# Optimization experiments

Measured on AMD Instinct MI355X. Metric: run time of the kernel, lower is better.

Reference implementation:

```python
import jax, jax.numpy as jnp
import numpy as np
from jax import lax

EPS = 1e-05
Q = 4          # window size (hard-coded in BotBlock)
HEADS = 4
DIM = 16       # bottleneck(64) // heads(4)


def conv3x3(x, w, b):
    # x: [N,C,H,W], w: [O,I,3,3]
    y = lax.conv_general_dilated(x, w, (1, 1), ((1, 1), (1, 1)),
                                 dimension_numbers=('NCHW', 'OIHW', 'NCHW'))
    return y + b[None, :, None, None]


def batchnorm(x, gamma, beta):
    # training-mode BN: batch statistics over (N,H,W), biased variance
    m = jnp.mean(x, axis=(0, 2, 3), keepdims=True)
    v = jnp.var(x, axis=(0, 2, 3), keepdims=True)
    xn = (x - m) * lax.rsqrt(v + EPS)
    return xn * gamma[None, :, None, None] + beta[None, :, None, None]


def rel_to_abs(x):
    # x: [B, H, L, 2L-1] -> [B, H, L, L] via pad/reshape trick
    B, H, L, _ = x.shape
    x = jnp.pad(x, ((0, 0), (0, 0), (0, 0), (0, 1)))          # [B,H,L,2L]
    flat = x.reshape(B, H, -1)                                  # [B,H,2L*L]
    flat = jnp.pad(flat, ((0, 0), (0, 0), (0, L - 1)))
    final = flat.reshape(B, H, L + 1, 2 * L - 1)
    return final[:, :, :L, L - 1:]                              # [B,H,L,L]


def relative_logits_1d(q, rel_k, perm):
    # q: [b, n, h, w, d], rel_k: [2w-1, d]
    b, n, h, w, d = q.shape
    rl = jnp.einsum('bnhwd,md->bnhwm', q, rel_k)
    rl = rl.reshape(b, n * h, w, 2 * w - 1)
    rl = rel_to_abs(rl)                                         # [b, n*h, w, w]
    rl = rl.reshape(b, n, h, w, w)
    rl = jnp.broadcast_to(rl[:, :, :, None], (b, n, h, h, w, w))
    return jnp.transpose(rl, perm)


def rel_pos_attention(q, k, v, rel_w, rel_h):
    # q,k,v: [b, heads, h, w, d]
    b, n, h, w, d = q.shape
    q = q * (d ** -0.5)
    logits = jnp.einsum('bnhwd,bnpqd->bnhwpq', q, k)
    logits = logits + relative_logits_1d(q, rel_w, (0, 1, 2, 4, 3, 5))
    logits = logits + relative_logits_1d(jnp.transpose(q, (0, 1, 3, 2, 4)),
                                         rel_h, (0, 1, 4, 2, 5, 3))
    weights = jax.nn.softmax(logits.reshape(b, n, h, w, h * w), axis=-1)
    weights = weights.reshape(b, n, h, w, h, w)
    out = jnp.einsum('bnhwpq,bnpqd->bhwnd', weights, v)         # [b,h,w,n,d]
    return out.reshape(b, h, w, n * d)                          # fold heads


def setup_inputs() -> dict:
    key = jax.random.key(0)
    ks = jax.random.split(key, 16)
    C_in, C_bot, C_out = 64, 64, 256
    inp = {
        'x': jax.random.normal(ks[0], (2, C_in, 256, 256), jnp.float32),
        'conv1_w': jax.random.normal(ks[1], (C_bot, C_in, 3, 3), jnp.float32) * 0.05,
        'conv1_b': jnp.zeros((C_bot,), jnp.float32),
        'bn1_g': jnp.ones((C_bot,), jnp.float32),
        'bn1_b': jnp.zeros((C_bot,), jnp.float32),
        'wq': jax.random.normal(ks[2], (C_bot, HEADS, DIM), jnp.float32) * 0.01,
        'wk': jax.random.normal(ks[3], (C_bot, HEADS, DIM), jnp.float32) * 0.01,
        'wv': jax.random.normal(ks[4], (C_bot, HEADS, DIM), jnp.float32) * 0.01,
        'rel_w': jax.random.normal(ks[5], (2 * Q - 1, DIM), jnp.float32) * (DIM ** -0.5),
        'rel_h': jax.random.normal(ks[6], (2 * Q - 1, DIM), jnp.float32) * (DIM ** -0.5),
        'bn2_g': jnp.ones((C_bot,), jnp.float32),
        'bn2_b': jnp.zeros((C_bot,), jnp.float32),
        'conv3_w': jax.random.normal(ks[7], (C_out, C_bot, 3, 3), jnp.float32) * 0.05,
        'conv3_b': jnp.zeros((C_out,), jnp.float32),
        # NOTE: original init_zero=True zeros bn3 gamma; we randomize it so the
        # output (and gradients) are non-trivial for kernel correctness checks.
        'bn3_g': jax.random.normal(ks[8], (C_out,), jnp.float32),
        'bn3_b': jnp.zeros((C_out,), jnp.float32),
    }
    return inp


def reference(x, conv1_w, conv1_b, bn1_g, bn1_b, wq, wk, wv, rel_w, rel_h,
              bn2_g, bn2_b, conv3_w, conv3_b, bn3_g, bn3_b):
    N, C, H, W = x.shape
    P_h, P_w = H // Q, W // Q
    # raw memory reinterpretation into 4x4 blocks (matches torch .reshape)
    xb = x.reshape(N * P_h * P_w, C, Q, Q)
    out = jax.nn.relu(batchnorm(conv3x3(xb, conv1_w, conv1_b), bn1_g, bn1_b))
    # GroupPointWise projections: NCHW -> NHWC then einsum
    feat = jnp.transpose(out, (0, 2, 3, 1))                     # [b,h,w,c]
    q = jnp.einsum('bhwc,cnp->bnhwp', feat, wq)
    k = jnp.einsum('bhwc,cnp->bnhwp', feat, wk)
    v = jnp.einsum('bhwc,cnp->bnhwp', feat, wv)
    o = rel_pos_attention(q, k, v, rel_w, rel_h)                # [b,h,w,c]
    o = jnp.transpose(o, (0, 3, 1, 2))                          # NCHW
    o = jax.nn.relu(batchnorm(o, bn2_g, bn2_b))
    o = batchnorm(conv3x3(o, conv3_w, conv3_b), bn3_g, bn3_b)   # no act
    C1 = o.shape[1]
    o = o.reshape(N, C1, H, W)
    return jax.nn.relu(o)
```

## Files before the change

### kernel.cpp

```cpp
#include <hip/hip_runtime.h>
#include <stdint.h>


#define EPSV 1e-5f
#define INV_N (1.0f / 131072.0f)

typedef unsigned short u16;
typedef __attribute__((ext_vector_type(8))) short short8b;
typedef __attribute__((ext_vector_type(4))) short short4b;
typedef __attribute__((ext_vector_type(4))) float f32x4;

__device__ __forceinline__ u16 f2bf(float f) {
  unsigned u = __float_as_uint(f);
  u += 0x7fffu + ((u >> 16) & 1u);
  return (u16)(u >> 16);
}
__device__ __forceinline__ float bf2f(u16 h) {
  return __uint_as_float((unsigned)h << 16);
}
__device__ __forceinline__ unsigned cvtpk(float lo, float hi) {
  unsigned r;
  asm("v_cvt_pk_bf16_f32 %0, %1, %2" : "=v"(r) : "v"(lo), "v"(hi));
  return r;
}
__device__ __forceinline__ short4b pack4(unsigned lo, unsigned hi) {
  union { unsigned u[2]; short4b s; } x;
  x.u[0] = lo; x.u[1] = hi;
  return x.s;
}
__device__ __forceinline__ f32x4 mfma16(short4b a, short4b b, f32x4 c) {
#if __has_builtin(__builtin_amdgcn_mfma_f32_16x16x16_bf16)
  return __builtin_amdgcn_mfma_f32_16x16x16_bf16(a, b, c, 0, 0, 0);
#elif __has_builtin(__builtin_amdgcn_mfma_f32_16x16x16bf16_1k)
  return __builtin_amdgcn_mfma_f32_16x16x16bf16_1k(a, b, c, 0, 0, 0);
#else
  f32x4 d;
  asm volatile("v_mfma_f32_16x16x16_bf16 %0, %1, %2, %3\n\ts_nop 7\n\ts_nop 7"
               : "=v"(d) : "v"(a), "v"(b), "v"(c));
  return d;
#endif
}

__device__ __forceinline__ float bn_scale(const float* __restrict__ acc,
                                          const float* __restrict__ gam,
                                          const float* __restrict__ bet,
                                          int C, int c, float& shift) {
  float S = acc[c], S2 = acc[C + c];
  float mean = S * INV_N;
  float var  = S2 * INV_N - mean * mean;
  float rstd = rsqrtf(var + EPSV);
  float sc = gam[c] * rstd;
  shift = bet[c] - mean * sc;
  return sc;
}

__global__ __launch_bounds__(256) void prep_kernel(const float* __restrict__ w1,
                                                   const float* __restrict__ w3,
                                                   const float* __restrict__ wq,
                                                   const float* __restrict__ wk,
                                                   const float* __restrict__ wv,
                                                   const float* __restrict__ relw,
                                                   const float* __restrict__ relh,
                                                   u16* __restrict__ wp1,
                                                   u16* __restrict__ wp3,
                                                   u16* __restrict__ wqkvT) {
  int i = blockIdx.x * 256 + threadIdx.x;
  const int tot1 = 18 * 64 * 40;
  const int tot3 = 9 * 256 * 64;
  if (i < tot1) {
    int ch = i / (64 * 40); int r = i - ch * 64 * 40; int o = r / 40; int kk = r - o * 40;
    float v = 0.f;
    if (kk < 32) { int k = ch * 32 + kk; int tap = k >> 6; int c = k & 63;
                   v = w1[o * 576 + c * 9 + tap]; }
    wp1[i] = f2bf(v);
  } else if (i < tot1 + tot3) {
    int j = i - tot1;
    int tap = j >> 14; int r = j & 16383; int o = r >> 6; int c = r & 63;
    wp3[j] = f2bf(w3[o * 576 + c * 9 + tap]);
  } else if (i < tot1 + tot3 + 192 * 64) {
    int j = i - tot1 - tot3;
    int oc = j >> 6, c = j & 63;
    const float* src = (oc < 64) ? wq : (oc < 128) ? wk : wv;
    float v = src[(c << 6) + (oc & 63)];
    if (oc < 64) v *= 0.25f;
    wqkvT[j] = f2bf(v);
  } else if (i < tot1 + tot3 + 192 * 64 + 4096) {
    int j = i - tot1 - tot3 - 192 * 64;
    int c = j & 63; int col = (j >> 6) & 31; int tbl = j >> 11;
    int n = col >> 3, m = col & 7;
    float v = 0.f;
    if (m < 7) {
      const float* rel = tbl ? relh : relw;
#pragma unroll
      for (int d = 0; d < 16; ++d) v += wq[c * 64 + n * 16 + d] * rel[m * 16 + d];
      v *= 0.25f;
    }
    wqkvT[(192 + tbl * 32 + col) * 64 + c] = f2bf(v);
  }
}

__global__ __launch_bounds__(256) void conv1_kernel(const float* __restrict__ x,
                                                    const u16* __restrict__ wp,
                                                    u16* __restrict__ bufb,
                                                    float* __restrict__ partials1) {
  __shared__ __align__(16) char featA[257 * 128];
  __shared__ __align__(16) char ldsW[2][64 * 80];
  const int t = threadIdx.x;
  const int lane = t & 63, w = t >> 6;
  const int lrow = lane & 15, lk = lane >> 4;
  const int wm = w >> 1, wn = w & 1;
  const size_t Mbase = (size_t)blockIdx.x * 256;

  int rel[9];
  {
    const int pi = lrow >> 2, pj = lrow & 3;
#pragma unroll
    for (int tap = 0; tap < 9; ++tap) {
      const int ti = tap / 3, tj = tap - ti * 3;
      int si = pi + ti - 1, sj = pj + tj - 1;
      bool valid = ((unsigned)si < 4u) && ((unsigned)sj < 4u);
      rel[tap] = valid ? ((si * 4 + sj) << 7) : (1 << 24);
    }
  }

  {
    const int cp = t >> 3, ph = t & 7;
    const int gsw = ((cp >> 2) << 4) | ((cp & 3) << 2);
#pragma unroll
    for (int i = 0; i < 16; ++i) {
      const float* bp = x + Mbase * 64 + i * 1024 + cp * 32 + ph * 2;
      float2 a = *reinterpret_cast<const float2*>(bp);
      float2 b = *reinterpret_cast<const float2*>(bp + 16);
#pragma unroll
      for (int j = 0; j < 2; ++j) {
        const int row = i * 16 + ph * 2 + j;
        unsigned pk = cvtpk(j ? a.y : a.x, j ? b.y : b.x);
        const int byte = row * 128 + (gsw ^ ((row & 7) << 4));
        *reinterpret_cast<unsigned*>(featA + byte) = pk;
      }
    }
  }
  if (t < 8) *reinterpret_cast<uint4*>(featA + 256 * 128 + t * 16) = uint4{0, 0, 0, 0};

  uint4 s0, s1;
  {
    const u16* sp = wp;
    s0 = *reinterpret_cast<const uint4*>(sp + (size_t)t * 8);
    if (t < 64) s1 = *reinterpret_cast<const uint4*>(sp + (size_t)(t + 256) * 8);
    *reinterpret_cast<uint4*>(ldsW[0] + t * 16) = s0;
    if (t < 64) *reinterpret_cast<uint4*>(ldsW[0] + (t + 256) * 16) = s1;
  }
  __syncthreads();

  f32x4 acc[8][2] = {};
#pragma unroll
  for (int chn = 0; chn < 18; ++chn) {
    const int cur = chn & 1;
    const int tap = chn >> 1, kk = chn & 1;
    if (chn + 1 < 18) {
      const u16* sp = wp + (chn + 1) * 2560;
      s0 = *reinterpret_cast<const uint4*>(sp + (size_t)t * 8);
      if (t < 64) s1 = *reinterpret_cast<const uint4*>(sp + (size_t)(t + 256) * 8);
    }
    const int kkg = (kk << 6) | (lk << 4);
    short8b bw[2];
#pragma unroll
    for (int n = 0; n < 2; ++n)
      bw[n] = *reinterpret_cast<const short8b*>(ldsW[cur] + (wn * 32 + n * 16 + lrow) * 80 + lk * 16);
#pragma unroll
    for (int m = 0; m < 8; ++m) {
      int ad = ((wm * 128 + m * 16) << 7) + rel[tap];
      ad = ad < 32768 ? ad : 32768;
      ad += (kkg ^ ((ad >> 3) & 0x70));
      short8b af = *reinterpret_cast<const short8b*>(featA + ad);
#pragma unroll
      for (int n = 0; n < 2; ++n)
        acc[m][n] = __builtin_amdgcn_mfma_f32_16x16x32_bf16(af, bw[n], acc[m][n], 0, 0, 0);
    }
    if (chn + 1 < 18) {
      *reinterpret_cast<uint4*>(ldsW[cur ^ 1] + t * 16) = s0;
      if (t < 64) *reinterpret_cast<uint4*>(ldsW[cur ^ 1] + (t + 256) * 16) = s1;
    }
    __syncthreads();
  }

#pragma unroll
  for (int m = 0; m < 8; ++m) {
    const size_t rowg0 = Mbase + wm * 128 + m * 16 + lk * 4;
#pragma unroll
    for (int n = 0; n < 2; ++n) {
      const int o = wn * 32 + n * 16 + lrow;
#pragma unroll
      for (int r = 0; r < 4; ++r)
        bufb[(rowg0 + r) * 64 + o] = f2bf(acc[m][n][r]);
    }
  }

  float* pst = reinterpret_cast<float*>(featA);
  if (t < 128) pst[t] = 0.f;
  __syncthreads();
#pragma unroll
  for (int n = 0; n < 2; ++n) {
    float s = 0.f, s2 = 0.f;
#pragma unroll
    for (int m = 0; m < 8; ++m)
#pragma unroll
      for (int r = 0; r < 4; ++r) {
        float v = acc[m][n][r];
        s += v; s2 = fmaf(v, v, s2);
      }
    s += __shfl_xor(s, 16); s2 += __shfl_xor(s2, 16);
    s += __shfl_xor(s, 32); s2 += __shfl_xor(s2, 32);
    if (lk == 0) {
      const int o = wn * 32 + n * 16 + lrow;
      atomicAdd(&pst[o], s);
      atomicAdd(&pst[64 + o], s2);
    }
  }
  __syncthreads();
  if (t < 128) partials1[(size_t)blockIdx.x * 128 + t] = pst[t];
}

__global__ __launch_bounds__(256) void reduce12_kernel(const float* __restrict__ p,
                                                       float* __restrict__ acc, int nrows) {
  const int c = blockIdx.x, t = threadIdx.x;
  float s = 0.f;
  for (int i = t; i < nrows; i += 256) s += p[(size_t)i * 128 + c];
#pragma unroll
  for (int off = 32; off > 0; off >>= 1) s += __shfl_down(s, off);
  __shared__ float red[4];
  if ((t & 63) == 0) red[t >> 6] = s;
  __syncthreads();
  if (t == 0) acc[c] = red[0] + red[1] + red[2] + red[3];
}

__global__ __launch_bounds__(256) void attn_kernel(u16* __restrict__ buf,
                                                   const u16* __restrict__ wqkvT,
                                                   const float* __restrict__ acc1,
                                                   const float* __restrict__ g1,
                                                   const float* __restrict__ b1,
                                                   float* __restrict__ partials2) {
  __shared__ float scsh[64][2];
  __shared__ float pstA[128];
  __shared__ __align__(16) u16 feat_l[4][1024];
  __shared__ __align__(16) float S_lds[4][16 * 18];
  __shared__ __align__(16) u16 V_lds[4][16 * 20];
  __shared__ __align__(16) float inv_lds[4][16];
  __shared__ __align__(16) u16 rLs[4][1152];
  const int t = threadIdx.x, u = t >> 6, lane = t & 63;
  const size_t b = (size_t)blockIdx.x * 4 + u;
  const int lrow = lane & 15, lk = lane >> 4;
  float* Sl = S_lds[u];
  u16* Vl = V_lds[u];
  float* invl = inv_lds[u];
  u16* rL = rLs[u];

  if (t < 64) {
    float sh; float sc = bn_scale(acc1, g1, b1, 64, t, sh);
    scsh[t][0] = sc; scsh[t][1] = sh;
  }
  if (t < 128) pstA[t] = 0.f;
  __syncthreads();

  {
    const int pos = lane >> 2, cq = lane & 3;
    const u16* src = buf + b * 1024 + pos * 64 + cq * 16;
    short8b v0 = *reinterpret_cast<const short8b*>(src);
    short8b v1 = *reinterpret_cast<const short8b*>(src + 8);
    float f[16];
#pragma unroll
    for (int j = 0; j < 8; ++j) {
      const int c0 = cq * 16 + j, c1 = cq * 16 + 8 + j;
      f[j]     = fmaxf(fmaf(bf2f((u16)v0[j]), scsh[c0][0], scsh[c0][1]), 0.f);
      f[8 + j] = fmaxf(fmaf(bf2f((u16)v1[j]), scsh[c1][0], scsh[c1][1]), 0.f);
    }
    uint4 q0{cvtpk(f[0], f[1]), cvtpk(f[2], f[3]), cvtpk(f[4], f[5]), cvtpk(f[6], f[7])};
    uint4 q1{cvtpk(f[8], f[9]), cvtpk(f[10], f[11]), cvtpk(f[12], f[13]), cvtpk(f[14], f[15])};
    const int g0 = (cq * 2) ^ (pos & 7), g1g = (cq * 2 + 1) ^ (pos & 7);
    *reinterpret_cast<uint4*>(&feat_l[u][pos * 64 + g0 * 8]) = q0;
    *reinterpret_cast<uint4*>(&feat_l[u][pos * 64 + g1g * 8]) = q1;
  }

  short8b bfeat[2];
#pragma unroll
  for (int ch = 0; ch < 2; ++ch) {
    const int kg = ch * 4 + lk;
    bfeat[ch] = *reinterpret_cast<const short8b*>(&feat_l[u][lrow * 64 + ((kg ^ (lrow & 7)) * 8)]);
  }
  short4b qf[4], kf[4];
  uint2 vf[4];
#pragma unroll
  for (int ct = 0; ct < 16; ++ct) {
    f32x4 d = {0.f, 0.f, 0.f, 0.f};
#pragma unroll
    for (int ch = 0; ch < 2; ++ch) {
      short8b wfr = *reinterpret_cast<const short8b*>(&wqkvT[(ct * 16 + lrow) * 64 + ch * 32 + lk * 8]);
      d = __builtin_amdgcn_mfma_f32_16x16x32_bf16(wfr, bfeat[ch], d, 0, 0, 0);
    }
    if (ct < 4) {
      qf[ct] = pack4(cvtpk(d[0], d[1]), cvtpk(d[2], d[3]));
    } else if (ct < 8) {
      kf[ct - 4] = pack4(cvtpk(d[0], d[1]), cvtpk(d[2], d[3]));
    } else if (ct < 12) {
      vf[ct - 8] = uint2{cvtpk(d[0], d[1]), cvtpk(d[2], d[3])};
    } else {
#pragma unroll
      for (int r = 0; r < 4; ++r) {
        const int rc = (ct - 12) * 16 + lk * 4 + r;
        const int tbl = rc >> 5, col = rc & 31;
        rL[tbl * 576 + (col >> 3) * 144 + lrow * 9 + (col & 7)] = f2bf(d[r]);
      }
    }
  }

  const f32x4 fzero = {0.f, 0.f, 0.f, 0.f};
  const int qj3 = 3 - (lrow & 3);
  const int qi = lrow >> 2;
#pragma unroll
  for (int n = 0; n < 4; ++n) {
    f32x4 S = mfma16(qf[n], kf[n], fzero);
#pragma unroll
    for (int r = 0; r < 4; ++r) Sl[(lk * 4 + r) * 18 + lrow] = S[r];
    const float* srow = Sl + lrow * 18 + lk * 4;
    float2 sa = *reinterpret_cast<const float2*>(srow);
    float2 sb = *reinterpret_cast<const float2*>(srow + 2);
    float s0 = sa.x, s1 = sa.y, s2 = sb.x, s3 = sb.y;
    const u16* rwp = rL + n * 144 + lrow * 9 + qj3;
    const float rh = bf2f(rL[576 + n * 144 + lrow * 9 + 3 + lk - qi]);
    s0 += bf2f(rwp[0]) + rh; s1 += bf2f(rwp[1]) + rh;
    s2 += bf2f(rwp[2]) + rh; s3 += bf2f(rwp[3]) + rh;
    float m = fmaxf(fmaxf(s0, s1), fmaxf(s2, s3));
    m = fmaxf(m, __shfl_xor(m, 16)); m = fmaxf(m, __shfl_xor(m, 32));
    float p0 = __expf(s0 - m), p1 = __expf(s1 - m);
    float p2 = __expf(s2 - m), p3 = __expf(s3 - m);
    float ls = p0 + p1 + p2 + p3;
    ls += __shfl_xor(ls, 16); ls += __shfl_xor(ls, 32);
    if (lk == 0) invl[lrow] = 1.f / ls;
    short4b pf = pack4(cvtpk(p0, p1), cvtpk(p2, p3));
    *reinterpret_cast<uint2*>(Vl + lrow * 20 + lk * 4) = vf[n];
    const int vb = lk * 4;
    unsigned v0 = Vl[(vb + 0) * 20 + lrow], v1 = Vl[(vb + 1) * 20 + lrow];
    unsigned v2 = Vl[(vb + 2) * 20 + lrow], v3 = Vl[(vb + 3) * 20 + lrow];
    short4b vB = pack4(v0 | (v1 << 16), v2 | (v3 << 16));
    f32x4 O = mfma16(pf, vB, fzero);
    float4 iv = *reinterpret_cast<const float4*>(invl + lk * 4);
    float o0 = O[0] * iv.x, o1 = O[1] * iv.y, o2 = O[2] * iv.z, o3 = O[3] * iv.w;
    u16* ob = buf + b * 1024 + (n << 4) + lrow;
    ob[(lk * 4 + 0) * 64] = f2bf(o0); ob[(lk * 4 + 1) * 64] = f2bf(o1);
    ob[(lk * 4 + 2) * 64] = f2bf(o2); ob[(lk * 4 + 3) * 64] = f2bf(o3);
    float ss = o0 + o1 + o2 + o3;
    float s2s = o0 * o0 + o1 * o1 + o2 * o2 + o3 * o3;
    ss += __shfl_xor(ss, 16); s2s += __shfl_xor(s2s, 16);
    ss += __shfl_xor(ss, 32); s2s += __shfl_xor(s2s, 32);
    if (lk == 0) {
      atomicAdd(&pstA[(n << 4) + lrow], ss);
      atomicAdd(&pstA[64 + (n << 4) + lrow], s2s);
    }
  }
  __syncthreads();
  if (t < 128) partials2[(size_t)blockIdx.x * 128 + t] = pstA[t];
}

__global__ __launch_bounds__(256, 2) void conv3_kernel(const u16* __restrict__ src,
                                                       const u16* __restrict__ wp,
                                                       const float* __restrict__ acc2,
                                                       const float* __restrict__ g2,
                                                       const float* __restrict__ b2,
                                                       u16* __restrict__ y3b,
                                                       float* __restrict__ partials3) {
  __shared__ __align__(16) u16 featB[257 * 64];
  __shared__ __align__(16) u16 ldsW[2][128 * 64];
  __shared__ float scsh[128];
  const int t = threadIdx.x;
  const int lane = t & 63, w = t >> 6;
  const int lrow = lane & 15, lk = lane >> 4;
  const int wm = w >> 1, wn = w & 1;
  const int Nbase = blockIdx.x * 256;
  const int ohalf = blockIdx.y;

  int rel[9];
  {
    const int pi = lrow >> 2, pj = lrow & 3;
#pragma unroll
    for (int tap = 0; tap < 9; ++tap) {
      const int ti = tap / 3, tj = tap - ti * 3;
      int si = pi + ti - 1, sj = pj + tj - 1;
      bool valid = ((unsigned)si < 4u) && ((unsigned)sj < 4u);
      rel[tap] = valid ? ((si * 4 + sj) << 7) : (1 << 24);
    }
  }
  if (t < 64) {
    float sh; float sc = bn_scale(acc2, g2, b2, 64, t, sh);
    scsh[t * 2] = sc; scsh[t * 2 + 1] = sh;
  }
  const int so = t >> 1, shalf = t & 1, so7 = so & 7;
  {
    const u16* wsrc = wp + ohalf * 8192 + so * 64 + shalf * 32;
    uint4 w0 = *reinterpret_cast<const uint4*>(wsrc);
    uint4 w1 = *reinterpret_cast<const uint4*>(wsrc + 8);
    uint4 w2 = *reinterpret_cast<const uint4*>(wsrc + 16);
    uint4 w3v = *reinterpret_cast<const uint4*>(wsrc + 24);
    char* dst = (char*)ldsW[0] + so * 128;
    const int gb = shalf * 4;
    *reinterpret_cast<uint4*>(dst + (((gb + 0) ^ so7) << 4)) = w0;
    *reinterpret_cast<uint4*>(dst + (((gb + 1) ^ so7) << 4)) = w1;
    *reinterpret_cast<uint4*>(dst + (((gb + 2) ^ so7) << 4)) = w2;
    *reinterpret_cast<uint4*>(dst + (((gb + 3) ^ so7) << 4)) = w3v;
  }
  __syncthreads();
  {
    const u16* srow = src + (size_t)(Nbase + t) * 64;
    char* drow = (char*)featB + t * 128;
    const int r7 = t & 7;
#pragma unroll
    for (int g = 0; g < 8; ++g) {
      short8b v = *reinterpret_cast<const short8b*>(srow + g * 8);
      float f[8];
#pragma unroll
      for (int j = 0; j < 8; ++j) {
        const int c = g * 8 + j;
        f[j] = fmaxf(fmaf(bf2f((u16)v[j]), scsh[c * 2], scsh[c * 2 + 1]), 0.f);
      }
      uint4 pk{cvtpk(f[0], f[1]), cvtpk(f[2], f[3]), cvtpk(f[4], f[5]), cvtpk(f[6], f[7])};
      *reinterpret_cast<uint4*>(drow + ((g ^ r7) << 4)) = pk;
    }
  }
  if (t < 8) *reinterpret_cast<uint4*>((char*)featB + 32768 + t * 16) = uint4{0, 0, 0, 0};
  uint4 r0, r1, r2, r3v;
  {
    const u16* wsrc = wp + 16384 + ohalf * 8192 + so * 64 + shalf * 32;
    r0 = *reinterpret_cast<const uint4*>(wsrc);
    r1 = *reinterpret_cast<const uint4*>(wsrc + 8);
    r2 = *reinterpret_cast<const uint4*>(wsrc + 16);
    r3v = *reinterpret_cast<const uint4*>(wsrc + 24);
  }
  __syncthreads();
  f32x4 acc[4][8] = {};
  const char* fB = (const char*)featB;
  const int swzA0 = (lk << 4) ^ ((lrow & 7) << 4);
  const int swzA1 = (64 | (lk << 4)) ^ ((lrow & 7) << 4);
#pragma unroll
  for (int tap = 0; tap < 9; ++tap) {
    const int cur = tap & 1;
    const char* lW = (const char*)ldsW[cur];
    short8b aw0[4], aw1[4];
#pragma unroll
    for (int m = 0; m < 4; ++m) {
      const int rowoff = (wm * 64 + m * 16 + lrow) << 7;
      aw0[m] = *reinterpret_cast<const short8b*>(lW + rowoff + swzA0);
      aw1[m] = *reinterpret_cast<const short8b*>(lW + rowoff + swzA1);
    }
#pragma unroll
    for (int n = 0; n < 8; ++n) {
      int ad0 = ((wn * 128 + n * 16) << 7) + rel[tap];
      ad0 = ad0 < 32768 ? ad0 : 32768;
      const int swz = (ad0 >> 3) & 0x70;
      short8b bf0 = *reinterpret_cast<const short8b*>(fB + ad0 + ((lk << 4) ^ swz));
      short8b bf1 = *reinterpret_cast<const short8b*>(fB + ad0 + ((64 | (lk << 4)) ^ swz));
#pragma unroll
      for (int m = 0; m < 4; ++m) {
        acc[m][n] = __builtin_amdgcn_mfma_f32_16x16x32_bf16(aw0[m], bf0, acc[m][n], 0, 0, 0);
        acc[m][n] = __builtin_amdgcn_mfma_f32_16x16x32_bf16(aw1[m], bf1, acc[m][n], 0, 0, 0);
      }
    }
    if (tap < 8) {
      char* dst = (char*)ldsW[cur ^ 1] + so * 128;
      const int gb = shalf * 4;
      *reinterpret_cast<uint4*>(dst + (((gb + 0) ^ so7) << 4)) = r0;
      *reinterpret_cast<uint4*>(dst + (((gb + 1) ^ so7) << 4)) = r1;
      *reinterpret_cast<uint4*>(dst + (((gb + 2) ^ so7) << 4)) = r2;
      *reinterpret_cast<uint4*>(dst + (((gb + 3) ^ so7) << 4)) = r3v;
      if (tap < 7) {
        const u16* wsrc = wp + (tap + 2) * 16384 + ohalf * 8192 + so * 64 + shalf * 32;
        r0 = *reinterpret_cast<const uint4*>(wsrc);
        r1 = *reinterpret_cast<const uint4*>(wsrc + 8);
        r2 = *reinterpret_cast<const uint4*>(wsrc + 16);
        r3v = *reinterpret_cast<const uint4*>(wsrc + 24);
      }
    }
    __syncthreads();
  }
#pragma unroll
  for (int m = 0; m < 4; ++m) {
    const int o = ohalf * 128 + wm * 64 + m * 16 + lk * 4;
#pragma unroll
    for (int n = 0; n < 8; ++n) {
      const int colg = Nbase + wn * 128 + n * 16 + lrow;
      const int b = colg >> 4, p = colg & 15;
      u16* dst = y3b + (size_t)b * 4096 + (size_t)o * 16 + p;
#pragma unroll
      for (int r = 0; r < 4; ++r) dst[r * 16] = f2bf(acc[m][n][r]);
    }
  }
  float* pst = reinterpret_cast<float*>(featB);
  pst[t] = 0.f;
  __syncthreads();
#pragma unroll
  for (int m = 0; m < 4; ++m) {
#pragma unroll
    for (int r = 0; r < 4; ++r) {
      float s = 0.f, s2 = 0.f;
#pragma unroll
      for (int n = 0; n < 8; ++n) {
        float v = acc[m][n][r];
        s += v; s2 = fmaf(v, v, s2);
      }
      s += __shfl_xor(s, 1); s2 += __shfl_xor(s2, 1);
      s += __shfl_xor(s, 2); s2 += __shfl_xor(s2, 2);
      s += __shfl_xor(s, 4); s2 += __shfl_xor(s2, 4);
      s += __shfl_xor(s, 8); s2 += __shfl_xor(s2, 8);
      if (lrow == 0) {
        const int ch = wm * 64 + m * 16 + lk * 4 + r;
        atomicAdd(&pst[ch], s);
        atomicAdd(&pst[128 + ch], s2);
      }
    }
  }
  __syncthreads();
  partials3[((size_t)(ohalf * 512 + blockIdx.x)) * 256 + t] = pst[t];
}

__global__ __launch_bounds__(256) void reduce3_kernel(const float* __restrict__ p,
                                                      float* __restrict__ acc3) {
  const int c2 = blockIdx.x, t = threadIdx.x;
  const int kind = c2 >> 8, c = c2 & 255;
  const int h = c >> 7, chl = c & 127;
  float s = 0.f;
  for (int i = t; i < 512; i += 256)
    s += p[((size_t)(h * 512 + i)) * 256 + kind * 128 + chl];
#pragma unroll
  for (int off = 32; off > 0; off >>= 1) s += __shfl_down(s, off);
  __shared__ float red[4];
  if ((t & 63) == 0) red[t >> 6] = s;
  __syncthreads();
  if (t == 0) acc3[kind * 256 + c] = red[0] + red[1] + red[2] + red[3];
}

__global__ __launch_bounds__(256) void final_kernel(const u16* __restrict__ y3b,
                                                    float* __restrict__ out,
                                                    const float* __restrict__ acc3,
                                                    const float* __restrict__ g3,
                                                    const float* __restrict__ b3) {
  const size_t i = ((size_t)blockIdx.x * 256 + threadIdx.x) * 8;
  const int c = (int)((i >> 4) & 255);
  float sh; const float sc = bn_scale(acc3, g3, b3, 256, c, sh);
  short8b v = *reinterpret_cast<const short8b*>(y3b + i);
  float4 o0, o1;
  o0.x = fmaxf(fmaf(bf2f((u16)v[0]), sc, sh), 0.f);
  o0.y = fmaxf(fmaf(bf2f((u16)v[1]), sc, sh), 0.f);
  o0.z = fmaxf(fmaf(bf2f((u16)v[2]), sc, sh), 0.f);
  o0.w = fmaxf(fmaf(bf2f((u16)v[3]), sc, sh), 0.f);
  o1.x = fmaxf(fmaf(bf2f((u16)v[4]), sc, sh), 0.f);
  o1.y = fmaxf(fmaf(bf2f((u16)v[5]), sc, sh), 0.f);
  o1.z = fmaxf(fmaf(bf2f((u16)v[6]), sc, sh), 0.f);
  o1.w = fmaxf(fmaf(bf2f((u16)v[7]), sc, sh), 0.f);
  *reinterpret_cast<float4*>(out + i) = o0;
  *reinterpret_cast<float4*>(out + i + 4) = o1;
}

extern "C" void kernel_launch(void* const* d_in, const int* in_sizes, int n_in,
                              void* d_out, int out_size, void* d_ws, size_t ws_size,
                              hipStream_t stream) {
  const float* x   = (const float*)d_in[0];
  const float* w1  = (const float*)d_in[1];
  const float* g1  = (const float*)d_in[3];
  const float* bb1 = (const float*)d_in[4];
  const float* wq  = (const float*)d_in[5];
  const float* wk  = (const float*)d_in[6];
  const float* wv  = (const float*)d_in[7];
  const float* rw  = (const float*)d_in[8];
  const float* rh  = (const float*)d_in[9];
  const float* g2  = (const float*)d_in[10];
  const float* bb2 = (const float*)d_in[11];
  const float* w3  = (const float*)d_in[12];
  const float* g3  = (const float*)d_in[14];
  const float* bb3 = (const float*)d_in[15];
  float* out = (float*)d_out;
  float* ws  = (float*)d_ws;

  u16*   bufb   = (u16*)ws;
  u16*   y3     = bufb + 8388608;
  u16*   wp1    = y3 + 33554432;
  u16*   wp3    = wp1 + 46080;
  u16*   wqkvT  = wp3 + 147456;
  float* acc1   = ws + 21076480;
  float* acc2   = acc1 + 128;
  float* acc3   = acc2 + 128;
  float* part1  = acc3 + 512;
  float* part2  = part1 + 65536;
  float* part3  = part2 + 262144;

  prep_kernel<<<820, 256, 0, stream>>>(w1, w3, wq, wk, wv, rw, rh, wp1, wp3, wqkvT);
  conv1_kernel<<<512, 256, 0, stream>>>(x, wp1, bufb, part1);
  reduce12_kernel<<<128, 256, 0, stream>>>(part1, acc1, 512);
  attn_kernel<<<2048, 256, 0, stream>>>(bufb, wqkvT, acc1, g1, bb1, part2);
  reduce12_kernel<<<128, 256, 0, stream>>>(part2, acc2, 2048);
  conv3_kernel<<<dim3(512, 2), 256, 0, stream>>>(bufb, wp3, acc2, g2, bb2, y3, part3);
  reduce3_kernel<<<512, 256, 0, stream>>>(part3, acc3);
  final_kernel<<<16384, 256, 0, stream>>>(y3, out, acc3, g3, bb3);
}
```

Measured before the change: 156.5 us.

## Replace partial-sum reduce kernels with global atomics and merge conv3 output halves

BatchNorm statistics are now accumulated with global float atomics directly into the accumulators, which removes the three separate reduce kernel launches and their partials buffers; a memset zeroes the accumulators first. conv3 now loops over both output-channel halves inside one block instead of using a 2-wide grid, so the feature tile is loaded into LDS once but each block does twice the work. The costs are atomic contention (e.g. 2048 blocks adding 128 values each in attn), nondeterministic summation order, and half as many conv3 blocks for parallelism.

```diff
diff --git a/kernel.cpp b/kernel.cpp
--- a/kernel.cpp
+++ b/kernel.cpp
@@ -102,7 +102,7 @@
 __global__ __launch_bounds__(256) void conv1_kernel(const float* __restrict__ x,
                                                     const u16* __restrict__ wp,
                                                     u16* __restrict__ bufb,
-                                                    float* __restrict__ partials1) {
+                                                    float* __restrict__ acc1) {
   __shared__ __align__(16) char featA[257 * 128];
   __shared__ __align__(16) char ldsW[2][64 * 80];
   const int t = threadIdx.x;
@@ -218,20 +218,7 @@
     }
   }
   __syncthreads();
-  if (t < 128) partials1[(size_t)blockIdx.x * 128 + t] = pst[t];
-}
-
-__global__ __launch_bounds__(256) void reduce12_kernel(const float* __restrict__ p,
-                                                       float* __restrict__ acc, int nrows) {
-  const int c = blockIdx.x, t = threadIdx.x;
-  float s = 0.f;
-  for (int i = t; i < nrows; i += 256) s += p[(size_t)i * 128 + c];
-#pragma unroll
-  for (int off = 32; off > 0; off >>= 1) s += __shfl_down(s, off);
-  __shared__ float red[4];
-  if ((t & 63) == 0) red[t >> 6] = s;
-  __syncthreads();
-  if (t == 0) acc[c] = red[0] + red[1] + red[2] + red[3];
+  if (t < 128) atomicAdd(&acc1[t], pst[t]);
 }
 
 __global__ __launch_bounds__(256) void attn_kernel(u16* __restrict__ buf,
@@ -239,7 +226,7 @@
                                                    const float* __restrict__ acc1,
                                                    const float* __restrict__ g1,
                                                    const float* __restrict__ b1,
-                                                   float* __restrict__ partials2) {
+                                                   float* __restrict__ acc2) {
   __shared__ float scsh[64][2];
   __shared__ float pstA[128];
   __shared__ __align__(16) u16 feat_l[4][1024];
@@ -358,7 +345,7 @@
     }
   }
   __syncthreads();
-  if (t < 128) partials2[(size_t)blockIdx.x * 128 + t] = pstA[t];
+  if (t < 128) atomicAdd(&acc2[t], pstA[t]);
 }
 
 __global__ __launch_bounds__(256, 2) void conv3_kernel(const u16* __restrict__ src,
@@ -367,7 +354,7 @@
                                                        const float* __restrict__ g2,
                                                        const float* __restrict__ b2,
                                                        u16* __restrict__ y3b,
-                                                       float* __restrict__ partials3) {
+                                                       float* __restrict__ acc3) {
   __shared__ __align__(16) u16 featB[257 * 64];
   __shared__ __align__(16) u16 ldsW[2][128 * 64];
   __shared__ float scsh[128];
@@ -376,7 +363,6 @@
   const int lrow = lane & 15, lk = lane >> 4;
   const int wm = w >> 1, wn = w & 1;
   const int Nbase = blockIdx.x * 256;
-  const int ohalf = blockIdx.y;
 
   int rel[9];
   {
@@ -393,21 +379,8 @@
     float sh; float sc = bn_scale(acc2, g2, b2, 64, t, sh);
     scsh[t * 2] = sc; scsh[t * 2 + 1] = sh;
   }
-  const int so = t >> 1, shalf = t & 1, so7 = so & 7;
-  {
-    const u16* wsrc = wp + ohalf * 8192 + so * 64 + shalf * 32;
-    uint4 w0 = *reinterpret_cast<const uint4*>(wsrc);
-    uint4 w1 = *reinterpret_cast<const uint4*>(wsrc + 8);
-    uint4 w2 = *reinterpret_cast<const uint4*>(wsrc + 16);
-    uint4 w3v = *reinterpret_cast<const uint4*>(wsrc + 24);
-    char* dst = (char*)ldsW[0] + so * 128;
-    const int gb = shalf * 4;
-    *reinterpret_cast<uint4*>(dst + (((gb + 0) ^ so7) << 4)) = w0;
-    *reinterpret_cast<uint4*>(dst + (((gb + 1) ^ so7) << 4)) = w1;
-    *reinterpret_cast<uint4*>(dst + (((gb + 2) ^ so7) << 4)) = w2;
-    *reinterpret_cast<uint4*>(dst + (((gb + 3) ^ so7) << 4)) = w3v;
-  }
   __syncthreads();
+
   {
     const u16* srow = src + (size_t)(Nbase + t) * 64;
     char* drow = (char*)featB + t * 128;
@@ -426,114 +399,119 @@
     }
   }
   if (t < 8) *reinterpret_cast<uint4*>((char*)featB + 32768 + t * 16) = uint4{0, 0, 0, 0};
-  uint4 r0, r1, r2, r3v;
-  {
-    const u16* wsrc = wp + 16384 + ohalf * 8192 + so * 64 + shalf * 32;
-    r0 = *reinterpret_cast<const uint4*>(wsrc);
-    r1 = *reinterpret_cast<const uint4*>(wsrc + 8);
-    r2 = *reinterpret_cast<const uint4*>(wsrc + 16);
-    r3v = *reinterpret_cast<const uint4*>(wsrc + 24);
-  }
-  __syncthreads();
-  f32x4 acc[4][8] = {};
+
   const char* fB = (const char*)featB;
   const int swzA0 = (lk << 4) ^ ((lrow & 7) << 4);
   const int swzA1 = (64 | (lk << 4)) ^ ((lrow & 7) << 4);
-#pragma unroll
-  for (int tap = 0; tap < 9; ++tap) {
-    const int cur = tap & 1;
-    const char* lW = (const char*)ldsW[cur];
-    short8b aw0[4], aw1[4];
+  const int so = t >> 1, shalf = t & 1, so7 = so & 7;
+
+  for (int oh = 0; oh < 2; ++oh) {
+    {
+      const u16* wsrc = wp + oh * 8192 + so * 64 + shalf * 32;
+      uint4 w0 = *reinterpret_cast<const uint4*>(wsrc);
+      uint4 w1 = *reinterpret_cast<const uint4*>(wsrc + 8);
+      uint4 w2 = *reinterpret_cast<const uint4*>(wsrc + 16);
+      uint4 w3v = *reinterpret_cast<const uint4*>(wsrc + 24);
+      char* dst = (char*)ldsW[0] + so * 128;
+      const int gb = shalf * 4;
+      *reinterpret_cast<uint4*>(dst + (((gb + 0) ^ so7) << 4)) = w0;
+      *reinterpret_cast<uint4*>(dst + (((gb + 1) ^ so7) << 4)) = w1;
+      *reinterpret_cast<uint4*>(dst + (((gb + 2) ^ so7) << 4)) = w2;
+      *reinterpret_cast<uint4*>(dst + (((gb + 3) ^ so7) << 4)) = w3v;
+    }
+    uint4 r0, r1, r2, r3v;
+    {
+      const u16* wsrc = wp + 16384 + oh * 8192 + so * 64 + shalf * 32;
+      r0 = *reinterpret_cast<const uint4*>(wsrc);
+      r1 = *reinterpret_cast<const uint4*>(wsrc + 8);
+      r2 = *reinterpret_cast<const uint4*>(wsrc + 16);
+      r3v = *reinterpret_cast<const uint4*>(wsrc + 24);
+    }
+    __syncthreads();
+
+    f32x4 acc[4][8];
+#pragma unroll
+    for (int m = 0; m < 4; ++m)
+#pragma unroll
+      for (int n = 0; n < 8; ++n) acc[m][n] = f32x4{0.f, 0.f, 0.f, 0.f};
+
+#pragma unroll
+    for (int tap = 0; tap < 9; ++tap) {
+      const int cur = tap & 1;
+      const char* lW = (const char*)ldsW[cur];
+      short8b aw0[4], aw1[4];
+#pragma unroll
+      for (int m = 0; m < 4; ++m) {
+        const int rowoff = (wm * 64 + m * 16 + lrow) << 7;
+        aw0[m] = *reinterpret_cast<const short8b*>(lW + rowoff + swzA0);
+        aw1[m] = *reinterpret_cast<const short8b*>(lW + rowoff + swzA1);
+      }
+#pragma unroll
+      for (int n = 0; n < 8; ++n) {
+        int ad0 = ((wn * 128 + n * 16) << 7) + rel[tap];
+        ad0 = ad0 < 32768 ? ad0 : 32768;
+        const int swz = (ad0 >> 3) & 0x70;
+        short8b bf0 = *reinterpret_cast<const short8b*>(fB + ad0 + ((lk << 4) ^ swz));
+        short8b bf1 = *reinterpret_cast<const short8b*>(fB + ad0 + ((64 | (lk << 4)) ^ swz));
+#pragma unroll
+        for (int m = 0; m < 4; ++m) {
+          acc[m][n] = __builtin_amdgcn_mfma_f32_16x16x32_bf16(aw0[m], bf0, acc[m][n], 0, 0, 0);
+          acc[m][n] = __builtin_amdgcn_mfma_f32_16x16x32_bf16(aw1[m], bf1, acc[m][n], 0, 0, 0);
+        }
+      }
+      if (tap < 8) {
+        char* dst = (char*)ldsW[cur ^ 1] + so * 128;
+        const int gb = shalf * 4;
+        *reinterpret_cast<uint4*>(dst + (((gb + 0) ^ so7) << 4)) = r0;
+        *reinterpret_cast<uint4*>(dst + (((gb + 1) ^ so7) << 4)) = r1;
+        *reinterpret_cast<uint4*>(dst + (((gb + 2) ^ so7) << 4)) = r2;
+        *reinterpret_cast<uint4*>(dst + (((gb + 3) ^ so7) << 4)) = r3v;
+        if (tap < 7) {
+          const u16* wsrc = wp + (tap + 2) * 16384 + oh * 8192 + so * 64 + shalf * 32;
+          r0 = *reinterpret_cast<const uint4*>(wsrc);
+          r1 = *reinterpret_cast<const uint4*>(wsrc + 8);
+          r2 = *reinterpret_cast<const uint4*>(wsrc + 16);
+          r3v = *reinterpret_cast<const uint4*>(wsrc + 24);
+        }
+      }
+      __syncthreads();
+    }
+
 #pragma unroll
     for (int m = 0; m < 4; ++m) {
-      const int rowoff = (wm * 64 + m * 16 + lrow) << 7;
-      aw0[m] = *reinterpret_cast<const short8b*>(lW + rowoff + swzA0);
-      aw1[m] = *reinterpret_cast<const short8b*>(lW + rowoff + swzA1);
-    }
-#pragma unroll
-    for (int n = 0; n < 8; ++n) {
-      int ad0 = ((wn * 128 + n * 16) << 7) + rel[tap];
-      ad0 = ad0 < 32768 ? ad0 : 32768;
-      const int swz = (ad0 >> 3) & 0x70;
-      short8b bf0 = *reinterpret_cast<const short8b*>(fB + ad0 + ((lk << 4) ^ swz));
-      short8b bf1 = *reinterpret_cast<const short8b*>(fB + ad0 + ((64 | (lk << 4)) ^ swz));
-#pragma unroll
-      for (int m = 0; m < 4; ++m) {
-        acc[m][n] = __builtin_amdgcn_mfma_f32_16x16x32_bf16(aw0[m], bf0, acc[m][n], 0, 0, 0);
-        acc[m][n] = __builtin_amdgcn_mfma_f32_16x16x32_bf16(aw1[m], bf1, acc[m][n], 0, 0, 0);
-      }
-    }
-    if (tap < 8) {
-      char* dst = (char*)ldsW[cur ^ 1] + so * 128;
-      const int gb = shalf * 4;
-      *reinterpret_cast<uint4*>(dst + (((gb + 0) ^ so7) << 4)) = r0;
-      *reinterpret_cast<uint4*>(dst + (((gb + 1) ^ so7) << 4)) = r1;
-      *reinterpret_cast<uint4*>(dst + (((gb + 2) ^ so7) << 4)) = r2;
-      *reinterpret_cast<uint4*>(dst + (((gb + 3) ^ so7) << 4)) = r3v;
-      if (tap < 7) {
-        const u16* wsrc = wp + (tap + 2) * 16384 + ohalf * 8192 + so * 64 + shalf * 32;
-        r0 = *reinterpret_cast<const uint4*>(wsrc);
-        r1 = *reinterpret_cast<const uint4*>(wsrc + 8);
-        r2 = *reinterpret_cast<const uint4*>(wsrc + 16);
-        r3v = *reinterpret_cast<const uint4*>(wsrc + 24);
-      }
-    }
-    __syncthreads();
-  }
-#pragma unroll
-  for (int m = 0; m < 4; ++m) {
-    const int o = ohalf * 128 + wm * 64 + m * 16 + lk * 4;
-#pragma unroll
-    for (int n = 0; n < 8; ++n) {
-      const int colg = Nbase + wn * 128 + n * 16 + lrow;
-      const int b = colg >> 4, p = colg & 15;
-      u16* dst = y3b + (size_t)b * 4096 + (size_t)o * 16 + p;
-#pragma unroll
-      for (int r = 0; r < 4; ++r) dst[r * 16] = f2bf(acc[m][n][r]);
-    }
-  }
-  float* pst = reinterpret_cast<float*>(featB);
-  pst[t] = 0.f;
-  __syncthreads();
-#pragma unroll
-  for (int m = 0; m < 4; ++m) {
-#pragma unroll
-    for (int r = 0; r < 4; ++r) {
-      float s = 0.f, s2 = 0.f;
+      const int o = oh * 128 + wm * 64 + m * 16 + lk * 4;
 #pragma unroll
       for (int n = 0; n < 8; ++n) {
-        float v = acc[m][n][r];
-        s += v; s2 = fmaf(v, v, s2);
-      }
-      s += __shfl_xor(s, 1); s2 += __shfl_xor(s2, 1);
-      s += __shfl_xor(s, 2); s2 += __shfl_xor(s2, 2);
-      s += __shfl_xor(s, 4); s2 += __shfl_xor(s2, 4);
-      s += __shfl_xor(s, 8); s2 += __shfl_xor(s2, 8);
-      if (lrow == 0) {
-        const int ch = wm * 64 + m * 16 + lk * 4 + r;
-        atomicAdd(&pst[ch], s);
-        atomicAdd(&pst[128 + ch], s2);
-      }
-    }
-  }
-  __syncthreads();
-  partials3[((size_t)(ohalf * 512 + blockIdx.x)) * 256 + t] = pst[t];
-}
-
-__global__ __launch_bounds__(256) void reduce3_kernel(const float* __restrict__ p,
-                                                      float* __restrict__ acc3) {
-  const int c2 = blockIdx.x, t = threadIdx.x;
-  const int kind = c2 >> 8, c = c2 & 255;
-  const int h = c >> 7, chl = c & 127;
-  float s = 0.f;
-  for (int i = t; i < 512; i += 256)
-    s += p[((size_t)(h * 512 + i)) * 256 + kind * 128 + chl];
-#pragma unroll
-  for (int off = 32; off > 0; off >>= 1) s += __shfl_down(s, off);
-  __shared__ float red[4];
-  if ((t & 63) == 0) red[t >> 6] = s;
-  __syncthreads();
-  if (t == 0) acc3[kind * 256 + c] = red[0] + red[1] + red[2] + red[3];
+        const int colg = Nbase + wn * 128 + n * 16 + lrow;
+        const int b = colg >> 4, p = colg & 15;
+        u16* dst = y3b + (size_t)b * 4096 + (size_t)o * 16 + p;
+#pragma unroll
+        for (int r = 0; r < 4; ++r) dst[r * 16] = f2bf(acc[m][n][r]);
+      }
+    }
+
+#pragma unroll
+    for (int m = 0; m < 4; ++m) {
+#pragma unroll
+      for (int r = 0; r < 4; ++r) {
+        float s = 0.f, s2 = 0.f;
+#pragma unroll
+        for (int n = 0; n < 8; ++n) {
+          float v = acc[m][n][r];
+          s += v; s2 = fmaf(v, v, s2);
+        }
+        s += __shfl_xor(s, 1); s2 += __shfl_xor(s2, 1);
+        s += __shfl_xor(s, 2); s2 += __shfl_xor(s2, 2);
+        s += __shfl_xor(s, 4); s2 += __shfl_xor(s2, 4);
+        s += __shfl_xor(s, 8); s2 += __shfl_xor(s2, 8);
+        if (lrow == 0) {
+          const int ch = oh * 128 + wm * 64 + m * 16 + lk * 4 + r;
+          atomicAdd(&acc3[ch], s);
+          atomicAdd(&acc3[256 + ch], s2);
+        }
+      }
+    }
+  }
 }
 
 __global__ __launch_bounds__(256) void final_kernel(const u16* __restrict__ y3b,
@@ -586,16 +564,11 @@
   float* acc1   = ws + 21076480;
   float* acc2   = acc1 + 128;
   float* acc3   = acc2 + 128;
-  float* part1  = acc3 + 512;
-  float* part2  = part1 + 65536;
-  float* part3  = part2 + 262144;
-
+
+  hipMemsetAsync(acc1, 0, 768 * sizeof(float), stream);
   prep_kernel<<<820, 256, 0, stream>>>(w1, w3, wq, wk, wv, rw, rh, wp1, wp3, wqkvT);
-  conv1_kernel<<<512, 256, 0, stream>>>(x, wp1, bufb, part1);
-  reduce12_kernel<<<128, 256, 0, stream>>>(part1, acc1, 512);
-  attn_kernel<<<2048, 256, 0, stream>>>(bufb, wqkvT, acc1, g1, bb1, part2);
-  reduce12_kernel<<<128, 256, 0, stream>>>(part2, acc2, 2048);
-  conv3_kernel<<<dim3(512, 2), 256, 0, stream>>>(bufb, wp3, acc2, g2, bb2, y3, part3);
-  reduce3_kernel<<<512, 256, 0, stream>>>(part3, acc3);
+  conv1_kernel<<<512, 256, 0, stream>>>(x, wp1, bufb, acc1);
+  attn_kernel<<<2048, 256, 0, stream>>>(bufb, wqkvT, acc1, g1, bb1, acc2);
+  conv3_kernel<<<512, 256, 0, stream>>>(bufb, wp3, acc2, g2, bb2, y3, acc3);
   final_kernel<<<16384, 256, 0, stream>>>(y3, out, acc3, g3, bb3);
 }
```

New measurement: 433.0 us. 2.77x slower.
